# Kernel tuning notes

Measured on AMD Instinct MI355X. Metric: run time of the kernel, lower is better.

Reference implementation:

```python
import jax, jax.numpy as jnp
import numpy as np

B, L, D, H = 4, 2048, 1024, 16
HD = D // H
EPS = 1e-5


def _layernorm(x, g, b):
    mu = jnp.mean(x, axis=-1, keepdims=True)
    var = jnp.mean(jnp.square(x - mu), axis=-1, keepdims=True)
    return (x - mu) * jax.lax.rsqrt(var + EPS) * g + b


def _rotate_half(x):
    x1, x2 = jnp.split(x, 2, axis=-1)
    return jnp.concatenate([-x2, x1], axis=-1)


def setup_inputs() -> dict:
    key = jax.random.key(0)
    ks = jax.random.split(key, 12)
    s = 0.02
    return {
        "x": jax.random.normal(ks[0], (B, L, D), jnp.float32),
        "pos_cos": jax.random.uniform(ks[1], (B, L, D), jnp.float32),
        "pos_sin": jax.random.uniform(ks[2], (B, L, D), jnp.float32),
        "attn_mask": jnp.zeros((B, L), jnp.float32),
        "Wq": jax.random.normal(ks[3], (D, D), jnp.float32) * s,
        "Wk": jax.random.normal(ks[4], (D, D), jnp.float32) * s,
        "Wv": jax.random.normal(ks[5], (D, D), jnp.float32) * s,
        "Wo": jax.random.normal(ks[6], (D, D), jnp.float32) * s,
        "W1": jax.random.normal(ks[7], (D, 2 * D), jnp.float32) * s,
        "W2": jax.random.normal(ks[8], (D, D), jnp.float32) * s,
        "g1": jnp.ones((D,), jnp.float32),
        "b1": jnp.zeros((D,), jnp.float32),
        "g2": jnp.ones((D,), jnp.float32),
        "b2": jnp.zeros((D,), jnp.float32),
    }


def reference(x, pos_cos, pos_sin, attn_mask, Wq, Wk, Wv, Wo, W1, W2, g1, b1, g2, b2):
    # --- attention sublayer (pre-LN) ---
    residual = x
    xn = _layernorm(x, g1, b1)
    split_heads = lambda t: t.reshape(B, L, H, HD).transpose(0, 2, 1, 3)  # [B,H,L,hd]
    q = split_heads(xn @ Wq)
    k = split_heads(xn @ Wk)
    v = split_heads(xn @ Wv)
    cos = split_heads(pos_cos)
    sin = split_heads(pos_sin)
    q = q * cos + _rotate_half(q) * sin
    k = k * cos + _rotate_half(k) * sin
    scores = jnp.einsum('bhqd,bhkd->bhqk', q, k) / np.float32(np.sqrt(HD))
    scores = scores + attn_mask[:, None, None, :]  # additive mask over keys
    probs = jax.nn.softmax(scores, axis=-1)
    ctx = jnp.einsum('bhqk,bhkd->bhqd', probs, v)
    ctx = ctx.transpose(0, 2, 1, 3).reshape(B, L, D)
    x = residual + ctx @ Wo
    # --- SwiGLU FFN sublayer (pre-LN) ---
    residual = x
    xn = _layernorm(x, g2, b2)
    h = xn @ W1
    x1, x2 = h[..., :D], h[..., D:]
    ffn = (jax.nn.silu(x1) * x2) @ W2
    return residual + ffn
```

## Files before the change

### kernel.cpp

```cpp
#include <hip/hip_runtime.h>
#include <hip/hip_bf16.h>

typedef unsigned short ushort_t;
typedef short short8 __attribute__((ext_vector_type(8)));
typedef unsigned short u16x4 __attribute__((ext_vector_type(4)));
typedef float f32x4 __attribute__((ext_vector_type(4)));
typedef int int2v __attribute__((ext_vector_type(2)));
typedef int int4v __attribute__((ext_vector_type(4)));

#define MFMA_BF16 __builtin_amdgcn_mfma_f32_16x16x32_bf16

#define GLDS16(g, l) __builtin_amdgcn_global_load_lds( \
    (__attribute__((address_space(1))) void*)(g), \
    (__attribute__((address_space(3))) void*)(l), 16, 0, 0)

#define WAITVM(n) asm volatile("s_waitcnt vmcnt(" #n ")" ::: "memory")

__device__ __forceinline__ unsigned short f2bf(float f) {
  union { float f; unsigned u; } v; v.f = f;
  unsigned r = v.u + 0x7FFFu + ((v.u >> 16) & 1u);
  return (unsigned short)(r >> 16);
}
__device__ __forceinline__ float bf2f(unsigned short h) {
  union { unsigned u; float f; } v; v.u = ((unsigned)h) << 16;
  return v.f;
}
__device__ __forceinline__ unsigned pack_bf2(float a, float b) {
  __hip_bfloat162 t = __float22bfloat162_rn(float2{a, b});
  union { __hip_bfloat162 h; unsigned u; } v; v.h = t;
  return v.u;
}
__device__ __forceinline__ float exp2_raw(float x) {
  float r;
  asm volatile("v_exp_f32 %0, %1" : "=v"(r) : "v"(x));
  return r;
}

#define BB 4
#define LL 2048
#define DD 1024
#define HH 16
#define HD 64
#define NROW (BB * LL)
#define LOG2E 1.4426950408889634f

template <int PERM>
__global__ __launch_bounds__(256) void wconv(const float* __restrict__ W,
                                             ushort_t* __restrict__ WT,
                                             int R, int C) {
  __shared__ float tile[32][33];
  const int ct = blockIdx.x * 32, rt = blockIdx.y * 32;
  const int tx = threadIdx.x & 31, ty = threadIdx.x >> 5;
#pragma unroll
  for (int j = 0; j < 4; ++j)
    tile[ty + j * 8][tx] = W[(size_t)(rt + ty + j * 8) * C + ct + tx];
  __syncthreads();
  int orow0 = ct;
  if (PERM)
    orow0 = (ct < 1024) ? ((ct >> 5) * 64) : ((((ct - 1024) >> 5) * 64) + 32);
#pragma unroll
  for (int j = 0; j < 4; ++j)
    WT[(size_t)(orow0 + ty + j * 8) * R + rt + tx] = f2bf(tile[tx][ty + j * 8]);
}

template <int BIN>
__global__ __launch_bounds__(256) void ln_kernel(const void* __restrict__ xin,
                                                 const float* __restrict__ g,
                                                 const float* __restrict__ bt,
                                                 ushort_t* __restrict__ out) {
  const int row = blockIdx.x, t = threadIdx.x;
  f32x4 v;
  if (BIN) {
    const u16x4 hv =
        *(const u16x4*)((const ushort_t*)xin + (size_t)row * DD + t * 4);
    v[0] = bf2f(hv[0]); v[1] = bf2f(hv[1]);
    v[2] = bf2f(hv[2]); v[3] = bf2f(hv[3]);
  } else {
    v = *(const f32x4*)((const float*)xin + (size_t)row * DD + t * 4);
  }
  float s = v[0] + v[1] + v[2] + v[3];
  float sq = v[0] * v[0] + v[1] * v[1] + v[2] * v[2] + v[3] * v[3];
#pragma unroll
  for (int off = 1; off < 64; off <<= 1) {
    s += __shfl_xor(s, off);
    sq += __shfl_xor(sq, off);
  }
  __shared__ float aw[4], aq[4];
  if ((t & 63) == 0) { aw[t >> 6] = s; aq[t >> 6] = sq; }
  __syncthreads();
  s = aw[0] + aw[1] + aw[2] + aw[3];
  sq = aq[0] + aq[1] + aq[2] + aq[3];
  const float mu = s * (1.f / DD);
  const float var = sq * (1.f / DD) - mu * mu;
  const float rs = rsqrtf(var + 1e-5f);
  u16x4 o;
#pragma unroll
  for (int j = 0; j < 4; ++j) {
    const int c = t * 4 + j;
    o[j] = f2bf((v[j] - mu) * rs * g[c] + bt[c]);
  }
  *(u16x4*)(out + (size_t)row * DD + t * 4) = o;
}

template <int EPI>
__global__ __launch_bounds__(256) void gemm_bt(const ushort_t* __restrict__ A,
                                               const ushort_t* __restrict__ BT,
                                               ushort_t* __restrict__ Cb,
                                               float* __restrict__ Cf,
                                               const float* __restrict__ residf,
                                               const ushort_t* __restrict__ residb,
                                               int M, int N, int K) {
  __shared__ ushort_t As[128 * 32];
  __shared__ ushort_t Bs[128 * 32];
  const int tid = threadIdx.x;
  const int lane = tid & 63;
  const int w = tid >> 6;
  const int wr = w >> 1, wc = w & 1;
  const int nwg = gridDim.x * gridDim.y;
  const int orig = blockIdx.y * gridDim.x + blockIdx.x;
  const int wg = (orig & 7) * (nwg >> 3) + (orig >> 3);
  const int bm = (wg / gridDim.x) * 128, bn = (wg % gridDim.x) * 128;
  const int lrow = lane >> 2;
  const int lcol = (lane & 3) * 8;
  const int fr = lane & 15;
  const int fo = (lane >> 4) * 8;
  f32x4 acc[4][4];
#pragma unroll
  for (int m = 0; m < 4; ++m)
#pragma unroll
    for (int n = 0; n < 4; ++n) acc[m][n] = (f32x4){0.f, 0.f, 0.f, 0.f};

  const int nk = K >> 5;
  for (int kt = 0; kt < nk; ++kt) {
    __syncthreads();
#pragma unroll
    for (int c = 0; c < 2; ++c) {
      const int seg = c * 4 + w;
      const int row = seg * 16 + lrow;
      GLDS16(A + (size_t)(bm + row) * K + kt * 32 + lcol, &As[seg * 512]);
      GLDS16(BT + (size_t)(bn + row) * K + kt * 32 + lcol, &Bs[seg * 512]);
    }
    asm volatile("s_waitcnt vmcnt(0)" ::: "memory");
    __syncthreads();
    short8 af[4], bf_[4];
#pragma unroll
    for (int m = 0; m < 4; ++m)
      af[m] = *(const short8*)&As[(wr * 64 + m * 16 + fr) * 32 + fo];
#pragma unroll
    for (int n = 0; n < 4; ++n)
      bf_[n] = *(const short8*)&Bs[(wc * 64 + n * 16 + fr) * 32 + fo];
#pragma unroll
    for (int m = 0; m < 4; ++m)
#pragma unroll
      for (int n = 0; n < 4; ++n)
        acc[m][n] = MFMA_BF16(af[m], bf_[n], acc[m][n], 0, 0, 0);
  }
  const int r0 = (lane >> 4) * 4;
#pragma unroll
  for (int m = 0; m < 4; ++m)
#pragma unroll
    for (int n = 0; n < 4; ++n)
#pragma unroll
      for (int r = 0; r < 4; ++r) {
        const int gr = bm + wr * 64 + m * 16 + r0 + r;
        const int gc = bn + wc * 64 + n * 16 + fr;
        const size_t o = (size_t)gr * N + gc;
        if (EPI == 1) Cb[o] = f2bf(residf[o] + acc[m][n][r]);
        else          Cf[o] = bf2f(residb[o]) + acc[m][n][r];
      }
}

template <int EPI>
__global__ __launch_bounds__(512, 2) void gemm8(
    const ushort_t* __restrict__ A, const ushort_t* __restrict__ BT,
    const float* __restrict__ pcos, const float* __restrict__ psin,
    ushort_t* __restrict__ qh, ushort_t* __restrict__ kh,
    ushort_t* __restrict__ vt, ushort_t* __restrict__ gact,
    int M, int N, int K) {
  __shared__ ushort_t SA[2][2][256 * 32];
  __shared__ ushort_t SB[2][2][256 * 32];
  const int tid = threadIdx.x, lane = tid & 63, w = tid >> 6;
  const int wm = w >> 2, wn = w & 3;
  const int nwg = gridDim.x * gridDim.y;
  const int orig = blockIdx.y * gridDim.x + blockIdx.x;
  const int wg = (orig & 7) * (nwg >> 3) + (orig >> 3);
  const int bm = (wg / gridDim.x) * 256, bn = (wg % gridDim.x) * 256;
  const int fr = lane & 15, hi = lane >> 4;
  const int NK = K >> 6;
  const int srow = lane >> 2;
  const int scol = ((lane & 3) ^ ((lane >> 4) & 2)) * 8;
  const int rdc = (hi ^ ((fr >> 2) & 2)) * 8;

  f32x4 acc[8][4];
#pragma unroll
  for (int m = 0; m < 8; ++m)
#pragma unroll
    for (int n = 0; n < 4; ++n) acc[m][n] = (f32x4){0.f, 0.f, 0.f, 0.f};

#define STAGE(gp, grow0, tile, kh_, slot)                                    \
  {                                                                          \
    const ushort_t* g0 = (gp) + (size_t)((grow0) + w * 16 + srow) * K +      \
                         (size_t)(tile) * 64 + (kh_) * 32 + scol;            \
    GLDS16(g0, (slot) + w * 512);                                            \
    GLDS16(g0 + (size_t)128 * K, (slot) + 4096 + w * 512);                   \
  }
#define LDA(dst, buf, kh_, mrep) \
  dst = *(const short8*)&SA[buf][kh_][(wm * 128 + (mrep) * 16 + fr) * 32 + rdc];
#define LDB(dst, buf, kh_, nrep) \
  dst = *(const short8*)&SB[buf][kh_][(wn * 64 + (nrep) * 16 + fr) * 32 + rdc];
#define QMFMA(NH)                                                            \
  __builtin_amdgcn_s_setprio(1);                                             \
  _Pragma("unroll") for (int m = 0; m < 8; ++m)                              \
      acc[m][2 * (NH)] =                                                     \
          MFMA_BF16(af[m], bfr[2 * (NH)], acc[m][2 * (NH)], 0, 0, 0);        \
  _Pragma("unroll") for (int m = 0; m < 8; ++m)                              \
      acc[m][2 * (NH) + 1] =                                                 \
          MFMA_BF16(af[m], bfr[2 * (NH) + 1], acc[m][2 * (NH) + 1], 0, 0, 0);\
  __builtin_amdgcn_s_setprio(0);

  STAGE(A, bm, 0, 0, &SA[0][0][0]);
  STAGE(BT, bn, 0, 0, &SB[0][0][0]);
  STAGE(A, bm, 0, 1, &SA[0][1][0]);
  STAGE(BT, bn, 0, 1, &SB[0][1][0]);
  STAGE(A, bm, 1, 0, &SA[1][0][0]);
  STAGE(BT, bn, 1, 0, &SB[1][0][0]);
  WAITVM(8);
  __builtin_amdgcn_s_barrier();

#pragma unroll 1
  for (int kt = 0; kt < NK; ++kt) {
    const int cur = kt & 1;
    short8 af[8], bfr[4];
    if (kt + 1 < NK) STAGE(A, bm, kt + 1, 1, &SA[(kt + 1) & 1][1][0]);
#pragma unroll
    for (int m = 0; m < 8; ++m) LDA(af[m], cur, 0, m);
    LDB(bfr[0], cur, 0, 0);
    LDB(bfr[1], cur, 0, 1);
    __builtin_amdgcn_s_barrier();
    QMFMA(0);
    __builtin_amdgcn_s_barrier();
    if (kt + 1 < NK) STAGE(BT, bn, kt + 1, 1, &SB[(kt + 1) & 1][1][0]);
    LDB(bfr[2], cur, 0, 2);
    LDB(bfr[3], cur, 0, 3);
    __builtin_amdgcn_s_barrier();
    QMFMA(1);
    if (kt + 1 < NK) { WAITVM(8); } else { WAITVM(0); }
    __builtin_amdgcn_s_barrier();
    if (kt + 2 < NK) STAGE(A, bm, kt + 2, 0, &SA[cur][0][0]);
#pragma unroll
    for (int m = 0; m < 8; ++m) LDA(af[m], cur, 1, m);
    LDB(bfr[0], cur, 1, 0);
    LDB(bfr[1], cur, 1, 1);
    __builtin_amdgcn_s_barrier();
    QMFMA(0);
    __builtin_amdgcn_s_barrier();
    if (kt + 2 < NK) STAGE(BT, bn, kt + 2, 0, &SB[cur][0][0]);
    LDB(bfr[2], cur, 1, 2);
    LDB(bfr[3], cur, 1, 3);
    __builtin_amdgcn_s_barrier();
    QMFMA(1);
    asm volatile("s_waitcnt lgkmcnt(0)" ::: "memory");
    if (kt + 2 < NK) { WAITVM(8); } else { WAITVM(4); }
    __builtin_amdgcn_s_barrier();
  }

  if (EPI == 1) {
    const int gcol = bn + wn * 64;
    const int region = gcol >> 10;
    const int h = (gcol & 1023) >> 6;
    const int b = bm >> 11;
    if (region < 2) {
      const float qs = (region == 0) ? 0.125f : 1.0f;
      ushort_t* dstbuf = (region == 0) ? qh : kh;
      const int dbase = h * 64;
#pragma unroll
      for (int m = 0; m < 8; ++m) {
        const int gr0 = bm + wm * 128 + m * 16 + hi * 4;
#pragma unroll
        for (int r = 0; r < 4; ++r) {
          const int gr = gr0 + r;
          const int l = gr & 2047;
          const float* pcr = pcos + (size_t)gr * DD + dbase;
          const float* psr = psin + (size_t)gr * DD + dbase;
          ushort_t* dst = dstbuf + ((size_t)(b * HH + h) * LL + l) * HD;
#pragma unroll
          for (int n = 0; n < 2; ++n) {
            const int dlo = n * 16 + fr;
            const float xlo = acc[m][n][r], xhi = acc[m][n + 2][r];
            dst[dlo] = f2bf((xlo * pcr[dlo] - xhi * psr[dlo]) * qs);
            dst[dlo + 32] = f2bf((xhi * pcr[dlo + 32] + xlo * psr[dlo + 32]) * qs);
          }
        }
      }
    } else {
      const size_t bhv = (size_t)(b * HH + h);
#pragma unroll
      for (int m = 0; m < 8; ++m) {
        const int l0 = (bm & 2047) + wm * 128 + m * 16;
        const int lt = l0 >> 6;
        const int slotb = 32 * ((m >> 1) & 1) + 8 * hi + 4 * (m & 1);
#pragma unroll
        for (int n = 0; n < 4; ++n) {
          const int hd = n * 16 + fr;
          u16x4 wv;
          wv[0] = f2bf(acc[m][n][0]);
          wv[1] = f2bf(acc[m][n][1]);
          wv[2] = f2bf(acc[m][n][2]);
          wv[3] = f2bf(acc[m][n][3]);
          *(u16x4*)(vt + (bhv * HD + hd) * LL + lt * 64 + slotb) = wv;
        }
      }
    }
  } else {
    const int jbase = ((bn + wn * 64) >> 6) * 32;
#pragma unroll
    for (int m = 0; m < 8; ++m) {
      const int gr0 = bm + wm * 128 + m * 16 + hi * 4;
#pragma unroll
      for (int r = 0; r < 4; ++r) {
        ushort_t* dst = gact + (size_t)(gr0 + r) * DD + jbase;
#pragma unroll
        for (int n = 0; n < 2; ++n) {
          const float x1 = acc[m][n][r];
          const float x2 = acc[m][n + 2][r];
          dst[n * 16 + fr] = f2bf(x1 / (1.f + __expf(-x1)) * x2);
        }
      }
    }
  }
#undef STAGE
#undef LDA
#undef LDB
#undef QMFMA
}

__global__ __launch_bounds__(512) void attn_kernel(
    const ushort_t* __restrict__ qh, const ushort_t* __restrict__ kh,
    const ushort_t* __restrict__ vt, const float* __restrict__ mask,
    ushort_t* __restrict__ ctx) {
  const int tid = threadIdx.x, lane = tid & 63, w = tid >> 6;
  const int bh = blockIdx.y, b = bh >> 4, h = bh & 15;
  const int q0 = blockIdx.x * 128;
  __shared__ ushort_t Ks[2][64 * 64];
  __shared__ ushort_t Vs[2][64 * 64];
  const int fr = lane & 15;
  const int hi = lane >> 4;
  const int fo = hi * 8;
  const int qrow = q0 + w * 16 + fr;
  const size_t qoff = ((size_t)bh * LL + qrow) * HD + fo;
  const short8 qf0 = *(const short8*)(qh + qoff);
  const short8 qf1 = *(const short8*)(qh + qoff + 32);
  short8 ones;
#pragma unroll
  for (int i = 0; i < 8; ++i) ones[i] = (short)0x3F80;

  f32x4 oacc[4];
  f32x4 lacc = (f32x4){0.f, 0.f, 0.f, 0.f};
#pragma unroll
  for (int m = 0; m < 4; ++m) oacc[m] = (f32x4){0.f, 0.f, 0.f, 0.f};

  const int lrow = lane >> 3;
  const int lcs = ((lane & 7) ^ lrow) * 8;

#define STAGE_KV(kt, bb)                                                      \
  {                                                                           \
    const int rr = w * 8 + lrow;                                              \
    GLDS16(kh + ((size_t)bh * LL + (kt) * 64 + rr) * HD + lcs,                \
           &Ks[bb][w * 512]);                                                 \
    GLDS16(vt + ((size_t)bh * HD + rr) * LL + (kt) * 64 + lcs,                \
           &Vs[bb][w * 512]);                                                 \
  }

  const float* mrow = mask + (size_t)b * LL;
  f32x4 mkc[4];
#pragma unroll
  for (int n = 0; n < 4; ++n)
    mkc[n] = *(const f32x4*)(mrow + n * 16 + hi * 4);

  STAGE_KV(0, 0);
  asm volatile("s_waitcnt vmcnt(0)" ::: "memory");
  __syncthreads();
  int cur = 0;
  const int NT = LL / 64;
  for (int kt = 0; kt < NT; ++kt) {
    f32x4 mkn[4];
    if (kt + 1 < NT) {
      STAGE_KV(kt + 1, cur ^ 1);
#pragma unroll
      for (int n = 0; n < 4; ++n)
        mkn[n] = *(const f32x4*)(mrow + (kt + 1) * 64 + n * 16 + hi * 4);
    } else {
#pragma unroll
      for (int n = 0; n < 4; ++n) mkn[n] = mkc[n];
    }

    f32x4 s[4];
#pragma unroll
    for (int n = 0; n < 4; ++n) s[n] = mkc[n];
    __builtin_amdgcn_s_setprio(1);
#pragma unroll
    for (int n = 0; n < 4; ++n) {
      const int krow = n * 16 + fr;
#pragma unroll
      for (int c = 0; c < 2; ++c) {
        const int col = (c * 32 + fo) ^ ((fr & 7) * 8);
        const short8 kf = *(const short8*)&Ks[cur][krow * 64 + col];
        s[n] = MFMA_BF16(kf, c ? qf1 : qf0, s[n], 0, 0, 0);
      }
    }
    __builtin_amdgcn_s_setprio(0);
    unsigned pk[4][2];
#pragma unroll
    for (int n = 0; n < 4; ++n) {
      const float p0 = exp2_raw(s[n][0] * LOG2E);
      const float p1 = exp2_raw(s[n][1] * LOG2E);
      const float p2 = exp2_raw(s[n][2] * LOG2E);
      const float p3 = exp2_raw(s[n][3] * LOG2E);
      pk[n][0] = pack_bf2(p0, p1);
      pk[n][1] = pack_bf2(p2, p3);
    }
    __builtin_amdgcn_s_setprio(1);
#pragma unroll
    for (int c = 0; c < 2; ++c) {
      int4v pw = {(int)pk[2 * c][0], (int)pk[2 * c][1],
                  (int)pk[2 * c + 1][0], (int)pk[2 * c + 1][1]};
      union { int4v i; short8 s; } pf; pf.i = pw;
#pragma unroll
      for (int m = 0; m < 4; ++m) {
        const int row = m * 16 + fr;
        const int col = (c * 32 + fo) ^ ((fr & 7) * 8);
        const short8 vf = *(const short8*)&Vs[cur][row * 64 + col];
        oacc[m] = MFMA_BF16(vf, pf.s, oacc[m], 0, 0, 0);
      }
      lacc = MFMA_BF16(ones, pf.s, lacc, 0, 0, 0);
    }
    __builtin_amdgcn_s_setprio(0);
#pragma unroll
    for (int n = 0; n < 4; ++n) mkc[n] = mkn[n];
    asm volatile("s_waitcnt vmcnt(0)" ::: "memory");
    __syncthreads();
    cur ^= 1;
  }
  const float inv = 1.f / lacc[0];
  const int q = q0 + w * 16 + fr;
  ushort_t* dst = ctx + ((size_t)b * LL + q) * DD + h * 64 + hi * 4;
#pragma unroll
  for (int m = 0; m < 4; ++m) {
    int2v val;
    val[0] = (int)pack_bf2(oacc[m][0] * inv, oacc[m][1] * inv);
    val[1] = (int)pack_bf2(oacc[m][2] * inv, oacc[m][3] * inv);
    *(int2v*)(dst + m * 16) = val;
  }
#undef STAGE_KV
}

extern "C" void kernel_launch(void* const* d_in, const int* in_sizes, int n_in,
                              void* d_out, int out_size, void* d_ws,
                              size_t ws_size, hipStream_t stream) {
  const float* x = (const float*)d_in[0];
  const float* pcos = (const float*)d_in[1];
  const float* psin = (const float*)d_in[2];
  const float* mask = (const float*)d_in[3];
  const float* Wq = (const float*)d_in[4];
  const float* Wk = (const float*)d_in[5];
  const float* Wv = (const float*)d_in[6];
  const float* Wo = (const float*)d_in[7];
  const float* W1 = (const float*)d_in[8];
  const float* W2 = (const float*)d_in[9];
  const float* g1 = (const float*)d_in[10];
  const float* b1 = (const float*)d_in[11];
  const float* g2 = (const float*)d_in[12];
  const float* b2 = (const float*)d_in[13];
  float* out = (float*)d_out;
  char* ws = (char*)d_ws;

  ushort_t* WQKVT = (ushort_t*)(ws);
  ushort_t* WOT = (ushort_t*)(ws + 6291456);
  ushort_t* W1T = (ushort_t*)(ws + 8388608);
  ushort_t* W2T = (ushort_t*)(ws + 12582912);
  ushort_t* XN = (ushort_t*)(ws + 14680064);
  ushort_t* GACT = (ushort_t*)(ws + 31457280 + 33554432);
  ushort_t* QH = (ushort_t*)(ws + 81788928);
  ushort_t* KH = (ushort_t*)(ws + 98566144);
  ushort_t* VT = (ushort_t*)(ws + 115343360);
  ushort_t* CTX = (ushort_t*)(ws + 132120576);
  ushort_t* XMIDB = (ushort_t*)(ws + 148897792);

  wconv<0><<<dim3(32, 32), 256, 0, stream>>>(Wq, WQKVT, 1024, 1024);
  wconv<0><<<dim3(32, 32), 256, 0, stream>>>(Wk, WQKVT + 1024 * 1024, 1024, 1024);
  wconv<0><<<dim3(32, 32), 256, 0, stream>>>(Wv, WQKVT + 2 * 1024 * 1024, 1024, 1024);
  wconv<0><<<dim3(32, 32), 256, 0, stream>>>(Wo, WOT, 1024, 1024);
  wconv<1><<<dim3(64, 32), 256, 0, stream>>>(W1, W1T, 1024, 2048);
  wconv<0><<<dim3(32, 32), 256, 0, stream>>>(W2, W2T, 1024, 1024);

  ln_kernel<0><<<NROW, 256, 0, stream>>>(x, g1, b1, XN);
  gemm8<1><<<dim3(12, 32), 512, 0, stream>>>(XN, WQKVT, pcos, psin, QH, KH, VT,
                                             nullptr, NROW, 3072, 1024);
  attn_kernel<<<dim3(16, 64), 512, 0, stream>>>(QH, KH, VT, mask, CTX);
  gemm_bt<1><<<dim3(8, 64), 256, 0, stream>>>(CTX, WOT, XMIDB, nullptr, x,
                                              nullptr, NROW, 1024, 1024);
  ln_kernel<1><<<NROW, 256, 0, stream>>>(XMIDB, g2, b2, XN);
  gemm8<2><<<dim3(8, 32), 512, 0, stream>>>(XN, W1T, nullptr, nullptr, nullptr,
                                            nullptr, nullptr, GACT, NROW, 2048,
                                            1024);
  gemm_bt<2><<<dim3(8, 64), 256, 0, stream>>>(GACT, W2T, nullptr, out, nullptr,
                                              XMIDB, NROW, 1024, 1024);
}
```

Baseline: 365.6 us.

## Replace pipelined 256x256 GEMM with simple 128x128 tiles and double attention query rows

The heavily pipelined 256x256 gemm8 kernel, with double-buffered LDS and interleaved barriers, is replaced by a simpler 128x128 tile kernel. It loads a single K=32 slice per iteration with a full vmcnt(0) wait, and its epilogues are reindexed for the smaller tile. Separately, each attention warp now processes two 16-row query strips, halving the attention grid so every K/V tile staged in LDS is reused across twice as many queries. The GEMM change gives up load/compute overlap and per-tile reuse in exchange for more blocks and less register pressure. The attention change raises register use per thread.

```diff
diff --git a/kernel.cpp b/kernel.cpp
--- a/kernel.cpp
+++ b/kernel.cpp
@@ -13,8 +13,6 @@
 #define GLDS16(g, l) __builtin_amdgcn_global_load_lds( \
     (__attribute__((address_space(1))) void*)(g), \
     (__attribute__((address_space(3))) void*)(l), 16, 0, 0)
-
-#define WAITVM(n) asm volatile("s_waitcnt vmcnt(" #n ")" ::: "memory")
 
 __device__ __forceinline__ unsigned short f2bf(float f) {
   union { float f; unsigned u; } v; v.f = f;
@@ -171,101 +169,61 @@
 }
 
 template <int EPI>
-__global__ __launch_bounds__(512, 2) void gemm8(
+__global__ __launch_bounds__(256) void gemm_f(
     const ushort_t* __restrict__ A, const ushort_t* __restrict__ BT,
     const float* __restrict__ pcos, const float* __restrict__ psin,
     ushort_t* __restrict__ qh, ushort_t* __restrict__ kh,
     ushort_t* __restrict__ vt, ushort_t* __restrict__ gact,
     int M, int N, int K) {
-  __shared__ ushort_t SA[2][2][256 * 32];
-  __shared__ ushort_t SB[2][2][256 * 32];
-  const int tid = threadIdx.x, lane = tid & 63, w = tid >> 6;
-  const int wm = w >> 2, wn = w & 3;
+  __shared__ ushort_t As[128 * 32];
+  __shared__ ushort_t Bs[128 * 32];
+  const int tid = threadIdx.x;
+  const int lane = tid & 63;
+  const int w = tid >> 6;
+  const int wr = w >> 1, wc = w & 1;
   const int nwg = gridDim.x * gridDim.y;
   const int orig = blockIdx.y * gridDim.x + blockIdx.x;
   const int wg = (orig & 7) * (nwg >> 3) + (orig >> 3);
-  const int bm = (wg / gridDim.x) * 256, bn = (wg % gridDim.x) * 256;
-  const int fr = lane & 15, hi = lane >> 4;
-  const int NK = K >> 6;
-  const int srow = lane >> 2;
-  const int scol = ((lane & 3) ^ ((lane >> 4) & 2)) * 8;
-  const int rdc = (hi ^ ((fr >> 2) & 2)) * 8;
-
-  f32x4 acc[8][4];
-#pragma unroll
-  for (int m = 0; m < 8; ++m)
+  const int bm = (wg / gridDim.x) * 128, bn = (wg % gridDim.x) * 128;
+  const int lrow = lane >> 2;
+  const int lcol = (lane & 3) * 8;
+  const int fr = lane & 15;
+  const int hi = lane >> 4;
+  const int fo = hi * 8;
+  f32x4 acc[4][4];
+#pragma unroll
+  for (int m = 0; m < 4; ++m)
 #pragma unroll
     for (int n = 0; n < 4; ++n) acc[m][n] = (f32x4){0.f, 0.f, 0.f, 0.f};
 
-#define STAGE(gp, grow0, tile, kh_, slot)                                    \
-  {                                                                          \
-    const ushort_t* g0 = (gp) + (size_t)((grow0) + w * 16 + srow) * K +      \
-                         (size_t)(tile) * 64 + (kh_) * 32 + scol;            \
-    GLDS16(g0, (slot) + w * 512);                                            \
-    GLDS16(g0 + (size_t)128 * K, (slot) + 4096 + w * 512);                   \
-  }
-#define LDA(dst, buf, kh_, mrep) \
-  dst = *(const short8*)&SA[buf][kh_][(wm * 128 + (mrep) * 16 + fr) * 32 + rdc];
-#define LDB(dst, buf, kh_, nrep) \
-  dst = *(const short8*)&SB[buf][kh_][(wn * 64 + (nrep) * 16 + fr) * 32 + rdc];
-#define QMFMA(NH)                                                            \
-  __builtin_amdgcn_s_setprio(1);                                             \
-  _Pragma("unroll") for (int m = 0; m < 8; ++m)                              \
-      acc[m][2 * (NH)] =                                                     \
-          MFMA_BF16(af[m], bfr[2 * (NH)], acc[m][2 * (NH)], 0, 0, 0);        \
-  _Pragma("unroll") for (int m = 0; m < 8; ++m)                              \
-      acc[m][2 * (NH) + 1] =                                                 \
-          MFMA_BF16(af[m], bfr[2 * (NH) + 1], acc[m][2 * (NH) + 1], 0, 0, 0);\
-  __builtin_amdgcn_s_setprio(0);
-
-  STAGE(A, bm, 0, 0, &SA[0][0][0]);
-  STAGE(BT, bn, 0, 0, &SB[0][0][0]);
-  STAGE(A, bm, 0, 1, &SA[0][1][0]);
-  STAGE(BT, bn, 0, 1, &SB[0][1][0]);
-  STAGE(A, bm, 1, 0, &SA[1][0][0]);
-  STAGE(BT, bn, 1, 0, &SB[1][0][0]);
-  WAITVM(8);
-  __builtin_amdgcn_s_barrier();
-
-#pragma unroll 1
-  for (int kt = 0; kt < NK; ++kt) {
-    const int cur = kt & 1;
-    short8 af[8], bfr[4];
-    if (kt + 1 < NK) STAGE(A, bm, kt + 1, 1, &SA[(kt + 1) & 1][1][0]);
-#pragma unroll
-    for (int m = 0; m < 8; ++m) LDA(af[m], cur, 0, m);
-    LDB(bfr[0], cur, 0, 0);
-    LDB(bfr[1], cur, 0, 1);
-    __builtin_amdgcn_s_barrier();
-    QMFMA(0);
-    __builtin_amdgcn_s_barrier();
-    if (kt + 1 < NK) STAGE(BT, bn, kt + 1, 1, &SB[(kt + 1) & 1][1][0]);
-    LDB(bfr[2], cur, 0, 2);
-    LDB(bfr[3], cur, 0, 3);
-    __builtin_amdgcn_s_barrier();
-    QMFMA(1);
-    if (kt + 1 < NK) { WAITVM(8); } else { WAITVM(0); }
-    __builtin_amdgcn_s_barrier();
-    if (kt + 2 < NK) STAGE(A, bm, kt + 2, 0, &SA[cur][0][0]);
-#pragma unroll
-    for (int m = 0; m < 8; ++m) LDA(af[m], cur, 1, m);
-    LDB(bfr[0], cur, 1, 0);
-    LDB(bfr[1], cur, 1, 1);
-    __builtin_amdgcn_s_barrier();
-    QMFMA(0);
-    __builtin_amdgcn_s_barrier();
-    if (kt + 2 < NK) STAGE(BT, bn, kt + 2, 0, &SB[cur][0][0]);
-    LDB(bfr[2], cur, 1, 2);
-    LDB(bfr[3], cur, 1, 3);
-    __builtin_amdgcn_s_barrier();
-    QMFMA(1);
-    asm volatile("s_waitcnt lgkmcnt(0)" ::: "memory");
-    if (kt + 2 < NK) { WAITVM(8); } else { WAITVM(4); }
-    __builtin_amdgcn_s_barrier();
+  const int nk = K >> 5;
+  for (int kt = 0; kt < nk; ++kt) {
+    __syncthreads();
+#pragma unroll
+    for (int c = 0; c < 2; ++c) {
+      const int seg = c * 4 + w;
+      const int row = seg * 16 + lrow;
+      GLDS16(A + (size_t)(bm + row) * K + kt * 32 + lcol, &As[seg * 512]);
+      GLDS16(BT + (size_t)(bn + row) * K + kt * 32 + lcol, &Bs[seg * 512]);
+    }
+    asm volatile("s_waitcnt vmcnt(0)" ::: "memory");
+    __syncthreads();
+    short8 af[4], bf_[4];
+#pragma unroll
+    for (int m = 0; m < 4; ++m)
+      af[m] = *(const short8*)&As[(wr * 64 + m * 16 + fr) * 32 + fo];
+#pragma unroll
+    for (int n = 0; n < 4; ++n)
+      bf_[n] = *(const short8*)&Bs[(wc * 64 + n * 16 + fr) * 32 + fo];
+#pragma unroll
+    for (int m = 0; m < 4; ++m)
+#pragma unroll
+      for (int n = 0; n < 4; ++n)
+        acc[m][n] = MFMA_BF16(af[m], bf_[n], acc[m][n], 0, 0, 0);
   }
 
   if (EPI == 1) {
-    const int gcol = bn + wn * 64;
+    const int gcol = bn + wc * 64;
     const int region = gcol >> 10;
     const int h = (gcol & 1023) >> 6;
     const int b = bm >> 11;
@@ -274,8 +232,8 @@
       ushort_t* dstbuf = (region == 0) ? qh : kh;
       const int dbase = h * 64;
 #pragma unroll
-      for (int m = 0; m < 8; ++m) {
-        const int gr0 = bm + wm * 128 + m * 16 + hi * 4;
+      for (int m = 0; m < 4; ++m) {
+        const int gr0 = bm + wr * 64 + m * 16 + hi * 4;
 #pragma unroll
         for (int r = 0; r < 4; ++r) {
           const int gr = gr0 + r;
@@ -294,11 +252,11 @@
       }
     } else {
       const size_t bhv = (size_t)(b * HH + h);
-#pragma unroll
-      for (int m = 0; m < 8; ++m) {
-        const int l0 = (bm & 2047) + wm * 128 + m * 16;
-        const int lt = l0 >> 6;
-        const int slotb = 32 * ((m >> 1) & 1) + 8 * hi + 4 * (m & 1);
+      const int l0 = (bm & 2047) + wr * 64;
+      const int lt = l0 >> 6;
+#pragma unroll
+      for (int m = 0; m < 4; ++m) {
+        const int slotb = 32 * (m >> 1) + 8 * hi + 4 * (m & 1);
 #pragma unroll
         for (int n = 0; n < 4; ++n) {
           const int hd = n * 16 + fr;
@@ -312,10 +270,10 @@
       }
     }
   } else {
-    const int jbase = ((bn + wn * 64) >> 6) * 32;
-#pragma unroll
-    for (int m = 0; m < 8; ++m) {
-      const int gr0 = bm + wm * 128 + m * 16 + hi * 4;
+    const int jbase = ((bn + wc * 64) >> 6) * 32;
+#pragma unroll
+    for (int m = 0; m < 4; ++m) {
+      const int gr0 = bm + wr * 64 + m * 16 + hi * 4;
 #pragma unroll
       for (int r = 0; r < 4; ++r) {
         ushort_t* dst = gact + (size_t)(gr0 + r) * DD + jbase;
@@ -328,10 +286,6 @@
       }
     }
   }
-#undef STAGE
-#undef LDA
-#undef LDB
-#undef QMFMA
 }
 
 __global__ __launch_bounds__(512) void attn_kernel(
@@ -340,24 +294,32 @@
     ushort_t* __restrict__ ctx) {
   const int tid = threadIdx.x, lane = tid & 63, w = tid >> 6;
   const int bh = blockIdx.y, b = bh >> 4, h = bh & 15;
-  const int q0 = blockIdx.x * 128;
+  const int q0 = blockIdx.x * 256;
   __shared__ ushort_t Ks[2][64 * 64];
   __shared__ ushort_t Vs[2][64 * 64];
   const int fr = lane & 15;
   const int hi = lane >> 4;
   const int fo = hi * 8;
-  const int qrow = q0 + w * 16 + fr;
-  const size_t qoff = ((size_t)bh * LL + qrow) * HD + fo;
-  const short8 qf0 = *(const short8*)(qh + qoff);
-  const short8 qf1 = *(const short8*)(qh + qoff + 32);
+  short8 qf[2][2];
+#pragma unroll
+  for (int st = 0; st < 2; ++st) {
+    const int qrow = q0 + w * 32 + st * 16 + fr;
+    const size_t qoff = ((size_t)bh * LL + qrow) * HD + fo;
+    qf[st][0] = *(const short8*)(qh + qoff);
+    qf[st][1] = *(const short8*)(qh + qoff + 32);
+  }
   short8 ones;
 #pragma unroll
   for (int i = 0; i < 8; ++i) ones[i] = (short)0x3F80;
 
-  f32x4 oacc[4];
-  f32x4 lacc = (f32x4){0.f, 0.f, 0.f, 0.f};
-#pragma unroll
-  for (int m = 0; m < 4; ++m) oacc[m] = (f32x4){0.f, 0.f, 0.f, 0.f};
+  f32x4 oacc[2][4];
+  f32x4 lacc[2];
+#pragma unroll
+  for (int st = 0; st < 2; ++st) {
+    lacc[st] = (f32x4){0.f, 0.f, 0.f, 0.f};
+#pragma unroll
+    for (int m = 0; m < 4; ++m) oacc[st][m] = (f32x4){0.f, 0.f, 0.f, 0.f};
+  }
 
   const int lrow = lane >> 3;
   const int lcs = ((lane & 7) ^ lrow) * 8;
@@ -394,62 +356,68 @@
       for (int n = 0; n < 4; ++n) mkn[n] = mkc[n];
     }
 
-    f32x4 s[4];
-#pragma unroll
-    for (int n = 0; n < 4; ++n) s[n] = mkc[n];
-    __builtin_amdgcn_s_setprio(1);
-#pragma unroll
-    for (int n = 0; n < 4; ++n) {
-      const int krow = n * 16 + fr;
+#pragma unroll
+    for (int st = 0; st < 2; ++st) {
+      f32x4 s[4];
+#pragma unroll
+      for (int n = 0; n < 4; ++n) s[n] = mkc[n];
+      __builtin_amdgcn_s_setprio(1);
+#pragma unroll
+      for (int n = 0; n < 4; ++n) {
+        const int krow = n * 16 + fr;
+#pragma unroll
+        for (int c = 0; c < 2; ++c) {
+          const int col = (c * 32 + fo) ^ ((fr & 7) * 8);
+          const short8 kf = *(const short8*)&Ks[cur][krow * 64 + col];
+          s[n] = MFMA_BF16(kf, qf[st][c], s[n], 0, 0, 0);
+        }
+      }
+      __builtin_amdgcn_s_setprio(0);
+      unsigned pk[4][2];
+#pragma unroll
+      for (int n = 0; n < 4; ++n) {
+        const float p0 = exp2_raw(s[n][0] * LOG2E);
+        const float p1 = exp2_raw(s[n][1] * LOG2E);
+        const float p2 = exp2_raw(s[n][2] * LOG2E);
+        const float p3 = exp2_raw(s[n][3] * LOG2E);
+        pk[n][0] = pack_bf2(p0, p1);
+        pk[n][1] = pack_bf2(p2, p3);
+      }
+      __builtin_amdgcn_s_setprio(1);
 #pragma unroll
       for (int c = 0; c < 2; ++c) {
-        const int col = (c * 32 + fo) ^ ((fr & 7) * 8);
-        const short8 kf = *(const short8*)&Ks[cur][krow * 64 + col];
-        s[n] = MFMA_BF16(kf, c ? qf1 : qf0, s[n], 0, 0, 0);
-      }
-    }
-    __builtin_amdgcn_s_setprio(0);
-    unsigned pk[4][2];
-#pragma unroll
-    for (int n = 0; n < 4; ++n) {
-      const float p0 = exp2_raw(s[n][0] * LOG2E);
-      const float p1 = exp2_raw(s[n][1] * LOG2E);
-      const float p2 = exp2_raw(s[n][2] * LOG2E);
-      const float p3 = exp2_raw(s[n][3] * LOG2E);
-      pk[n][0] = pack_bf2(p0, p1);
-      pk[n][1] = pack_bf2(p2, p3);
-    }
-    __builtin_amdgcn_s_setprio(1);
-#pragma unroll
-    for (int c = 0; c < 2; ++c) {
-      int4v pw = {(int)pk[2 * c][0], (int)pk[2 * c][1],
-                  (int)pk[2 * c + 1][0], (int)pk[2 * c + 1][1]};
-      union { int4v i; short8 s; } pf; pf.i = pw;
-#pragma unroll
-      for (int m = 0; m < 4; ++m) {
-        const int row = m * 16 + fr;
-        const int col = (c * 32 + fo) ^ ((fr & 7) * 8);
-        const short8 vf = *(const short8*)&Vs[cur][row * 64 + col];
-        oacc[m] = MFMA_BF16(vf, pf.s, oacc[m], 0, 0, 0);
-      }
-      lacc = MFMA_BF16(ones, pf.s, lacc, 0, 0, 0);
-    }
-    __builtin_amdgcn_s_setprio(0);
+        int4v pw = {(int)pk[2 * c][0], (int)pk[2 * c][1],
+                    (int)pk[2 * c + 1][0], (int)pk[2 * c + 1][1]};
+        union { int4v i; short8 s; } pf; pf.i = pw;
+#pragma unroll
+        for (int m = 0; m < 4; ++m) {
+          const int row = m * 16 + fr;
+          const int col = (c * 32 + fo) ^ ((fr & 7) * 8);
+          const short8 vf = *(const short8*)&Vs[cur][row * 64 + col];
+          oacc[st][m] = MFMA_BF16(vf, pf.s, oacc[st][m], 0, 0, 0);
+        }
+        lacc[st] = MFMA_BF16(ones, pf.s, lacc[st], 0, 0, 0);
+      }
+      __builtin_amdgcn_s_setprio(0);
+    }
 #pragma unroll
     for (int n = 0; n < 4; ++n) mkc[n] = mkn[n];
     asm volatile("s_waitcnt vmcnt(0)" ::: "memory");
     __syncthreads();
     cur ^= 1;
   }
-  const float inv = 1.f / lacc[0];
-  const int q = q0 + w * 16 + fr;
-  ushort_t* dst = ctx + ((size_t)b * LL + q) * DD + h * 64 + hi * 4;
-#pragma unroll
-  for (int m = 0; m < 4; ++m) {
-    int2v val;
-    val[0] = (int)pack_bf2(oacc[m][0] * inv, oacc[m][1] * inv);
-    val[1] = (int)pack_bf2(oacc[m][2] * inv, oacc[m][3] * inv);
-    *(int2v*)(dst + m * 16) = val;
+#pragma unroll
+  for (int st = 0; st < 2; ++st) {
+    const float inv = 1.f / lacc[st][0];
+    const int q = q0 + w * 32 + st * 16 + fr;
+    ushort_t* dst = ctx + ((size_t)b * LL + q) * DD + h * 64 + hi * 4;
+#pragma unroll
+    for (int m = 0; m < 4; ++m) {
+      int2v val;
+      val[0] = (int)pack_bf2(oacc[st][m][0] * inv, oacc[st][m][1] * inv);
+      val[1] = (int)pack_bf2(oacc[st][m][2] * inv, oacc[st][m][3] * inv);
+      *(int2v*)(dst + m * 16) = val;
+    }
   }
 #undef STAGE_KV
 }
@@ -494,15 +462,15 @@
   wconv<0><<<dim3(32, 32), 256, 0, stream>>>(W2, W2T, 1024, 1024);
 
   ln_kernel<0><<<NROW, 256, 0, stream>>>(x, g1, b1, XN);
-  gemm8<1><<<dim3(12, 32), 512, 0, stream>>>(XN, WQKVT, pcos, psin, QH, KH, VT,
-                                             nullptr, NROW, 3072, 1024);
-  attn_kernel<<<dim3(16, 64), 512, 0, stream>>>(QH, KH, VT, mask, CTX);
+  gemm_f<1><<<dim3(24, 64), 256, 0, stream>>>(XN, WQKVT, pcos, psin, QH, KH,
+                                              VT, nullptr, NROW, 3072, 1024);
+  attn_kernel<<<dim3(8, 64), 512, 0, stream>>>(QH, KH, VT, mask, CTX);
   gemm_bt<1><<<dim3(8, 64), 256, 0, stream>>>(CTX, WOT, XMIDB, nullptr, x,
                                               nullptr, NROW, 1024, 1024);
   ln_kernel<1><<<NROW, 256, 0, stream>>>(XMIDB, g2, b2, XN);
-  gemm8<2><<<dim3(8, 32), 512, 0, stream>>>(XN, W1T, nullptr, nullptr, nullptr,
-                                            nullptr, nullptr, GACT, NROW, 2048,
-                                            1024);
+  gemm_f<2><<<dim3(16, 64), 256, 0, stream>>>(XN, W1T, nullptr, nullptr,
+                                              nullptr, nullptr, nullptr, GACT,
+                                              NROW, 2048, 1024);
   gemm_bt<2><<<dim3(8, 64), 256, 0, stream>>>(GACT, W2T, nullptr, out, nullptr,
                                               XMIDB, NROW, 1024, 1024);
 }
```

After: 377.4 us. 3.2% more time.
